# Optimization experiments

Measured on AMD Instinct MI355X. Metric: run time of the kernel, lower is better.

## Reference

```python
import jax, jax.numpy as jnp
import numpy as np

N = 100_000      # nodes
E = 400_000      # edges
NPERM = 100_000  # local receptive-field subgraphs
L = 16           # lrp_length
H = 64           # hid_dim
NLAYERS = 4
G = 1024         # graphs in the batch
P = NPERM * L    # permutation rows (must be NPERM * L)


def _spmm(row, col, val, mat, m):
    # COO sparse [m, n] @ dense [n, d]  (torch_sparse.spmm equivalent)
    return jax.ops.segment_sum(val[:, None] * mat[col], row, num_segments=m)


def setup_inputs() -> dict:
    key = jax.random.key(0)
    ks = jax.random.split(key, 16)
    inp = {}
    inp["node_feat"] = jax.random.normal(ks[0], (N, 28), jnp.float32)
    inp["degs"] = jax.random.uniform(ks[1], (N,), jnp.float32) * 8.0
    inp["batch"] = jnp.sort(jax.random.randint(ks[2], (N,), 0, G)).astype(jnp.int32)
    # node -> perm-length permutation matrix (one nonzero per perm row)
    inp["n2p_row"] = jnp.arange(P, dtype=jnp.int32)
    inp["n2p_col"] = jax.random.randint(ks[3], (P,), 0, N, dtype=jnp.int32)
    inp["n2p_val"] = jnp.ones((P,), jnp.float32)
    # edge -> perm-length permutation matrix
    inp["e2p_row"] = jnp.arange(P, dtype=jnp.int32)
    inp["e2p_col"] = jax.random.randint(ks[4], (P,), 0, E, dtype=jnp.int32)
    inp["e2p_val"] = jnp.ones((P,), jnp.float32)
    # pooling matrix: subgraph row -> root node, shape [N, NPERM]
    inp["pool_row"] = jax.random.randint(ks[5], (NPERM,), 0, N, dtype=jnp.int32)
    inp["pool_col"] = jnp.arange(NPERM, dtype=jnp.int32)
    inp["pool_val"] = jax.random.uniform(ks[6], (NPERM,), jnp.float32)
    # parameters
    inp["atom_W"] = jax.random.normal(ks[7], (28, H), jnp.float32) * 0.1
    inp["atom_b"] = jnp.zeros((H,), jnp.float32)
    inp["edge_W"] = jax.random.normal(ks[8], (1, H), jnp.float32) * 0.1
    inp["edge_b"] = jnp.zeros((H,), jnp.float32)
    inp["W_lrp"] = jax.random.normal(ks[9], (NLAYERS, H, H, L), jnp.float32) * 0.03
    inp["b_lrp"] = jnp.zeros((NLAYERS, H), jnp.float32)
    inp["dn0_W"] = jax.random.normal(ks[10], (NLAYERS, 1, 2 * H), jnp.float32) * 0.2
    inp["dn0_b"] = jnp.zeros((NLAYERS, 2 * H), jnp.float32)
    inp["dn1_W"] = jax.random.normal(ks[11], (NLAYERS, 2 * H, H), jnp.float32) * 0.1
    inp["dn1_b"] = jnp.zeros((NLAYERS, H), jnp.float32)
    return inp


def reference(node_feat, degs, batch,
              n2p_row, n2p_col, n2p_val,
              e2p_row, e2p_col, e2p_val,
              pool_row, pool_col, pool_val,
              atom_W, atom_b, edge_W, edge_b,
              W_lrp, b_lrp, dn0_W, dn0_b, dn1_W, dn1_b):
    x = node_feat @ atom_W + atom_b                       # atom_encoder  [N, H]
    # all edge features are 1 -> edge_encoder gives identical rows
    efeat = jnp.ones((E, 1), node_feat.dtype) @ edge_W + edge_b  # [E, H]
    for i in range(NLAYERS):
        # gather nodes + edges into perm-length layout   [P, H]
        perm = _spmm(n2p_row, n2p_col, n2p_val, x, P) \
             + _spmm(e2p_row, e2p_col, e2p_val, efeat, P)
        # transpose(0,1).view(H,-1,L).permute(1,2,0) == reshape(NPERM, L, H)
        t = perm.reshape(NPERM, L, H)
        # einsum('dab,bca->dc') with weights [H_in, H_out, L]
        h = jax.nn.relu(jnp.einsum('plh,hcl->pc', t, W_lrp[i]) + b_lrp[i])  # [NPERM, H]
        pooled = _spmm(pool_row, pool_col, pool_val, h, N)  # [N, H]
        hid = jax.nn.relu(degs[:, None] @ dn0_W[i] + dn0_b[i])  # [N, 2H]
        factor = hid @ dn1_W[i] + dn1_b[i]                      # [N, H]
        x = pooled * factor
    # global mean pool over graphs
    sums = jax.ops.segment_sum(x, batch, num_segments=G)
    cnts = jax.ops.segment_sum(jnp.ones((x.shape[0],), x.dtype), batch, num_segments=G)
    return sums / jnp.maximum(cnts, 1.0)[:, None]
```

## Files before the change

### kernel.cpp

```cpp
#include <hip/hip_runtime.h>

typedef __attribute__((ext_vector_type(8))) short bf16x8;
typedef __attribute__((ext_vector_type(4))) float f32x4;

#define N_NODES   100000
#define NPERM_    100000
#define L_        16
#define G_        1024
#define CAP_      20
#define OVF_MAX   4096

__device__ inline unsigned short f32_to_bf16(float f) {
    unsigned u = __float_as_uint(f);
    unsigned r = (u + 0x7fff + ((u >> 16) & 1)) >> 16;
    return (unsigned short)r;
}
__device__ inline float bflo(unsigned u) { return __uint_as_float(u << 16); }
__device__ inline float bfhi(unsigned u) { return __uint_as_float(u & 0xffff0000u); }
__device__ inline float bfup(unsigned short s) { return __uint_as_float((unsigned)s << 16); }
__device__ inline unsigned pk2(float a, float b) {
    return (unsigned)f32_to_bf16(a) | ((unsigned)f32_to_bf16(b) << 16);
}

typedef __attribute__((address_space(1))) const unsigned int gas_u32;
typedef __attribute__((address_space(3))) unsigned int las_u32;
__device__ __forceinline__ void gld16(const void* g, void* l) {
    __builtin_amdgcn_global_load_lds((gas_u32*)g, (las_u32*)l, 16, 0, 0);
}

__global__ __launch_bounds__(256) void k_prep_w(const float* __restrict__ W,
                                                unsigned short* __restrict__ Wt2) {
    int o = blockIdx.x * 256 + threadIdx.x;
    int j    = o & 7;
    int lane = (o >> 3) & 63;
    int sc   = (o >> 9) & 7;
    int l    = (o >> 12) & 15;
    int ho   = (o >> 16) & 1;
    int i    = o >> 17;
    int s = sc >> 2, cb = sc & 3;
    int k = s * 32 + (lane >> 4) * 8 + j;
    int c = cb * 16 + (lane & 15);
    float f = W[(((i * 64 + k) * 64) + c) * 16 + l];
    unsigned short hh = f32_to_bf16(f);
    Wt2[o] = ho ? f32_to_bf16(f - bfup(hh)) : hh;
}

__global__ __launch_bounds__(256) void k_prep_factor(const float* __restrict__ dn0_W,
                                                     const float* __restrict__ dn0_b,
                                                     const float* __restrict__ dn1_W,
                                                     const float* __restrict__ dn1_b,
                                                     float* __restrict__ tab,
                                                     float* __restrict__ thr) {
    int i     = blockIdx.x;
    int chunk = blockIdx.y;
    int tid   = threadIdx.x;
    __shared__ float A[128], B[128], ts[128], tv[128];
    __shared__ float W1l[128 * 64];
    if (tid < 128) { A[tid] = dn0_W[i * 128 + tid]; B[tid] = dn0_b[i * 128 + tid]; }
    {
        const float4* src = (const float4*)(dn1_W + (size_t)i * 8192);
        float4*       dst = (float4*)W1l;
        for (int t = tid; t < 2048; t += 256) dst[t] = src[t];
    }
    __syncthreads();
    if (tid < 128) {
        float a = A[tid], b = B[tid];
        float tj = -b / a;
        if (a == 0.f || !(tj > 0.f)) tj = 1e30f;
        tv[tid] = tj;
    }
    __syncthreads();
    if (tid < 128) {
        float tj = tv[tid];
        int rank = 0;
        for (int j = 0; j < 128; ++j) {
            float o = tv[j];
            rank += (o < tj) || (o == tj && j < tid);
        }
        ts[rank] = tj;
    }
    __syncthreads();
    if (chunk == 0 && tid < 128) thr[i * 128 + tid] = ts[tid];
    int s0 = chunk * 17;
    int s1 = min(s0 + 17, 129);
    float* tb = tab + (size_t)i * 129 * 128;
    for (int item = s0 * 64 + tid; item < s1 * 64; item += 256) {
        int s = item >> 6;
        int c = item & 63;
        float lo = (s == 0) ? 0.f : ts[s - 1];
        float hi = (s == 128) ? 1e30f : ts[s];
        float g;
        if (lo > 1e29f)       g = 1e29f;
        else if (hi > 1e29f)  g = lo + 1.f;
        else                  g = 0.5f * (lo + hi);
        float alpha = 0.f, beta = dn1_b[i * 64 + c];
        for (int j = 0; j < 128; ++j) {
            if (fmaf(g, A[j], B[j]) > 0.f) {
                float w1 = W1l[j * 64 + c];
                alpha = fmaf(A[j], w1, alpha);
                beta  = fmaf(B[j], w1, beta);
            }
        }
        tb[s * 128 + c * 2 + 0] = alpha;
        tb[s * 128 + c * 2 + 1] = beta;
    }
}

__global__ __launch_bounds__(256) void k_atom(const float* __restrict__ feat,
                                              const float* __restrict__ W,
                                              const float* __restrict__ b,
                                              unsigned short* __restrict__ xb) {
    __shared__ float Wlds[28 * 64];
    __shared__ float blds[64];
    int tid = threadIdx.x;
    for (int t = tid; t < 28 * 64; t += 256) Wlds[t] = W[t];
    if (tid < 64) blds[tid] = b[tid];
    __syncthreads();
    int n = blockIdx.x * 4 + (tid >> 6);
    int c = tid & 63;
    if (n >= N_NODES) return;
    const float* fr = feat + n * 28;
    float acc = blds[c];
#pragma unroll
    for (int j = 0; j < 28; ++j) acc = fmaf(fr[j], Wlds[j * 64 + c], acc);
    xb[n * 64 + c] = f32_to_bf16(acc);
}

__global__ __launch_bounds__(256) void k_bucket(const int* __restrict__ prow,
                                                int* __restrict__ cntn,
                                                int* __restrict__ bucket,
                                                int* __restrict__ ovf,
                                                int* __restrict__ ovfc) {
    int d = blockIdx.x * 256 + threadIdx.x;
    if (d >= NPERM_) return;
    int n = prow[d];
    int s = atomicAdd(cntn + n, 1);
    if (s < CAP_) bucket[n * CAP_ + s] = d;
    else { int o = atomicAdd(ovfc, 1); if (o < OVF_MAX) ovf[o] = d; }
}

__global__ __launch_bounds__(256, 3) void k_lrp(const unsigned short* __restrict__ xbuf,
                                                const int*   __restrict__ n2p_col,
                                                const float* __restrict__ n2p_val,
                                                const float* __restrict__ e2p_val,
                                                const float* __restrict__ edge_W,
                                                const float* __restrict__ edge_b,
                                                const unsigned short* __restrict__ Wt2,
                                                const float* __restrict__ bl,
                                                unsigned short* __restrict__ hout) {
    __shared__ unsigned short Tb[2][4][2][512];
    __shared__ unsigned short Wb[2][2][8][512];
    int tid = threadIdx.x;
    int lane = tid & 63;
    int w = tid >> 6;
    int r = lane & 15, q = lane >> 4;
    int d0 = blockIdx.x * 64;
    int myrow = w * 16 + r;
    int dg = min(d0 + myrow, NPERM_ - 1);
    size_t pbase = (size_t)dg * 16;

    float efr[2][8];
#pragma unroll
    for (int s = 0; s < 2; ++s) {
        int kb = s * 32 + q * 8;
        float4 wa = *(const float4*)(edge_W + kb);
        float4 wc = *(const float4*)(edge_W + kb + 4);
        float4 ba = *(const float4*)(edge_b + kb);
        float4 bc = *(const float4*)(edge_b + kb + 4);
        efr[s][0] = wa.x + ba.x; efr[s][1] = wa.y + ba.y;
        efr[s][2] = wa.z + ba.z; efr[s][3] = wa.w + ba.w;
        efr[s][4] = wc.x + bc.x; efr[s][5] = wc.y + bc.y;
        efr[s][6] = wc.z + bc.z; efr[s][7] = wc.w + bc.w;
    }

    f32x4 acc[4];
#pragma unroll
    for (int cb = 0; cb < 4; ++cb) acc[cb] = (f32x4)0.f;

    auto stage = [&](int l, int buf, int col) {
        const unsigned short* ap = xbuf + (size_t)col * 64 + q * 8;
        gld16(ap,      &Tb[buf][w][0][0]);
        gld16(ap + 32, &Tb[buf][w][1][0]);
        const unsigned short* wl = Wt2 + l * 4096;
#pragma unroll
        for (int i = 0; i < 4; ++i) {
            int c = w * 4 + i;
            gld16(wl + (c >> 3) * 65536 + (c & 7) * 512 + lane * 8,
                  &Wb[buf][c >> 3][c & 7][0]);
        }
    };

    int colA = n2p_col[pbase + 0];
    stage(0, 0, colA);
    colA = n2p_col[pbase + 1];
    float vnC = n2p_val[pbase + 0], veC = e2p_val[pbase + 0];
    __syncthreads();

#pragma unroll 1
    for (int l = 0; l < L_; ++l) {
        int buf = l & 1;
        if (l < 15) stage(l + 1, buf ^ 1, colA);
        if (l < 14) colA = n2p_col[pbase + l + 2];
        float vn = vnC, ve = veC;
        if (l < 15) { vnC = n2p_val[pbase + l + 1]; veC = e2p_val[pbase + l + 1]; }
#pragma unroll
        for (int s = 0; s < 2; ++s) {
            uint4 v = *(const uint4*)&Tb[buf][w][s][lane * 8];
            uint4 aw;
            aw.x = pk2(fmaf(vn, bflo(v.x), ve * efr[s][0]),
                       fmaf(vn, bfhi(v.x), ve * efr[s][1]));
            aw.y = pk2(fmaf(vn, bflo(v.y), ve * efr[s][2]),
                       fmaf(vn, bfhi(v.y), ve * efr[s][3]));
            aw.z = pk2(fmaf(vn, bflo(v.z), ve * efr[s][4]),
                       fmaf(vn, bfhi(v.z), ve * efr[s][5]));
            aw.w = pk2(fmaf(vn, bflo(v.w), ve * efr[s][6]),
                       fmaf(vn, bfhi(v.w), ve * efr[s][7]));
            bf16x8 a0 = *(bf16x8*)&aw;
#pragma unroll
            for (int cb = 0; cb < 4; ++cb) {
                bf16x8 bh = *(const bf16x8*)&Wb[buf][0][s * 4 + cb][lane * 8];
                bf16x8 bo = *(const bf16x8*)&Wb[buf][1][s * 4 + cb][lane * 8];
                acc[cb] = __builtin_amdgcn_mfma_f32_16x16x32_bf16(a0, bh, acc[cb], 0, 0, 0);
                acc[cb] = __builtin_amdgcn_mfma_f32_16x16x32_bf16(a0, bo, acc[cb], 0, 0, 0);
            }
        }
        __syncthreads();
    }

    {
        unsigned short* F = &Tb[0][0][0][0] + w * 1024;
#pragma unroll
        for (int cb = 0; cb < 4; ++cb) {
            float bias = bl[cb * 16 + r];
#pragma unroll
            for (int reg = 0; reg < 4; ++reg)
                F[(q * 4 + reg) * 64 + cb * 16 + r] =
                    f32_to_bf16(fmaxf(acc[cb][reg] + bias, 0.f));
        }
#pragma unroll
        for (int ii = 0; ii < 2; ++ii) {
            int idx = lane + ii * 64;
            uint4 v = ((const uint4*)F)[idx];
            int R = d0 + w * 16 + (idx >> 3);
            if (R < NPERM_)
                *(uint4*)(hout + (size_t)R * 64 + (idx & 7) * 8) = v;
        }
    }
}

__global__ __launch_bounds__(256) void k_pool_seg(const unsigned short* __restrict__ h,
                                                  const int*   __restrict__ cntn,
                                                  const int*   __restrict__ bucket,
                                                  const int*   __restrict__ ovf,
                                                  const int*   __restrict__ ovfc,
                                                  const int*   __restrict__ prow,
                                                  const float* __restrict__ pval,
                                                  const float* __restrict__ degs,
                                                  const float* __restrict__ tab,
                                                  const float* __restrict__ thr,
                                                  float* __restrict__ x,
                                                  unsigned short* __restrict__ xbo,
                                                  int last) {
    __shared__ float thrl[128];
    int tid = threadIdx.x;
    if (tid < 128) thrl[tid] = thr[tid];
    __syncthreads();
    int n  = blockIdx.x * 16 + (tid >> 4);
    int c4 = (tid & 15) * 4;
    if (n >= N_NODES) return;
    float dgv = degs[n];
    int seg = 0;
    if (thrl[63]       < dgv) seg = 64;
    if (thrl[seg + 31] < dgv) seg += 32;
    if (thrl[seg + 15] < dgv) seg += 16;
    if (thrl[seg + 7]  < dgv) seg += 8;
    if (thrl[seg + 3]  < dgv) seg += 4;
    if (thrl[seg + 1]  < dgv) seg += 2;
    if (thrl[seg]      < dgv) seg += 1;
    float4 p = make_float4(0.f, 0.f, 0.f, 0.f);
    int cn = min(cntn[n], CAP_);
    for (int j = 0; j < cn; ++j) {
        int   d  = bucket[n * CAP_ + j];
        float pv = pval[d];
        ushort4 hv = *(const ushort4*)(h + (size_t)d * 64 + c4);
        p.x = fmaf(pv, bfup(hv.x), p.x);
        p.y = fmaf(pv, bfup(hv.y), p.y);
        p.z = fmaf(pv, bfup(hv.z), p.z);
        p.w = fmaf(pv, bfup(hv.w), p.w);
    }
    int novf = *ovfc;
    if (novf > 0) {
        int ne = novf < OVF_MAX ? novf : OVF_MAX;
        for (int e = 0; e < ne; ++e) {
            int d = ovf[e];
            if (prow[d] == n) {
                float pv = pval[d];
                ushort4 hv = *(const ushort4*)(h + (size_t)d * 64 + c4);
                p.x = fmaf(pv, bfup(hv.x), p.x);
                p.y = fmaf(pv, bfup(hv.y), p.y);
                p.z = fmaf(pv, bfup(hv.z), p.z);
                p.w = fmaf(pv, bfup(hv.w), p.w);
            }
        }
    }
    const float4* tf = (const float4*)(tab + (size_t)(seg * 64 + c4) * 2);
    float4 t0 = tf[0], t1 = tf[1];
    float4 xo;
    xo.x = p.x * fmaf(t0.x, dgv, t0.y);
    xo.y = p.y * fmaf(t0.z, dgv, t0.w);
    xo.z = p.z * fmaf(t1.x, dgv, t1.y);
    xo.w = p.w * fmaf(t1.z, dgv, t1.w);
    if (last) {
        *(float4*)(x + (size_t)n * 64 + c4) = xo;
    } else {
        ushort4 s;
        s.x = f32_to_bf16(xo.x); s.y = f32_to_bf16(xo.y);
        s.z = f32_to_bf16(xo.z); s.w = f32_to_bf16(xo.w);
        *(ushort4*)(xbo + (size_t)n * 64 + c4) = s;
    }
}

__global__ __launch_bounds__(256) void k_gpool(const float* __restrict__ x,
                                               const int* __restrict__ batch,
                                               float* __restrict__ out,
                                               float* __restrict__ cnt) {
    int wave = (blockIdx.x * 256 + threadIdx.x) >> 6;
    int lane = threadIdx.x & 63;
    int n0 = wave * 64;
    if (n0 >= N_NODES) return;
    int n1 = min(n0 + 64, N_NODES);
    int g = batch[n0];
    float s = 0.f, c = 0.f;
    for (int n = n0; n < n1; ++n) {
        int gn = batch[n];
        if (gn != g) {
            atomicAdd(out + (size_t)g * 64 + lane, s);
            if (lane == 0) atomicAdd(cnt + g, c);
            s = 0.f; c = 0.f; g = gn;
        }
        s += x[(size_t)n * 64 + lane];
        c += 1.f;
    }
    atomicAdd(out + (size_t)g * 64 + lane, s);
    if (lane == 0) atomicAdd(cnt + g, c);
}

__global__ __launch_bounds__(256) void k_gdiv(float* __restrict__ out,
                                              const float* __restrict__ cnt) {
    int idx = blockIdx.x * 256 + threadIdx.x;
    if (idx >= G_ * 64) return;
    out[idx] /= fmaxf(cnt[idx >> 6], 1.f);
}

extern "C" void kernel_launch(void* const* d_in, const int* in_sizes, int n_in,
                              void* d_out, int out_size, void* d_ws, size_t ws_size,
                              hipStream_t stream) {
    const float* node_feat = (const float*)d_in[0];
    const float* degs      = (const float*)d_in[1];
    const int*   batch     = (const int*)  d_in[2];
    const int*   n2p_col   = (const int*)  d_in[4];
    const float* n2p_val   = (const float*)d_in[5];
    const float* e2p_val   = (const float*)d_in[8];
    const int*   pool_row  = (const int*)  d_in[9];
    const float* pool_val  = (const float*)d_in[11];
    const float* atom_W    = (const float*)d_in[12];
    const float* atom_b    = (const float*)d_in[13];
    const float* edge_W    = (const float*)d_in[14];
    const float* edge_b    = (const float*)d_in[15];
    const float* W_lrp     = (const float*)d_in[16];
    const float* b_lrp     = (const float*)d_in[17];
    const float* dn0_W     = (const float*)d_in[18];
    const float* dn0_b     = (const float*)d_in[19];
    const float* dn1_W     = (const float*)d_in[20];
    const float* dn1_b     = (const float*)d_in[21];

    char* ws = (char*)d_ws;
    unsigned short* h      = (unsigned short*)(ws);
    unsigned short* xb     = (unsigned short*)(ws + 12800000);
    unsigned short* Wt2    = (unsigned short*)(ws + 25600000);
    int*            bucket = (int*)           (ws + 26648576);
    int*            cntn   = (int*)           (ws + 34648576);
    int*            ovf    = (int*)           (ws + 35048576);
    int*            ovfc   = (int*)           (ws + 35064960);
    float*          tab    = (float*)         (ws + 35065088);
    float*          thr    = (float*)         (ws + 35329280);
    float*          cntg   = (float*)         (ws + 35331328);
    float*          x      = (float*)         (ws + 35335424);

    hipLaunchKernelGGL(k_prep_w, dim3(2048), dim3(256), 0, stream, W_lrp, Wt2);
    hipLaunchKernelGGL(k_prep_factor, dim3(4, 8), dim3(256), 0, stream,
                       dn0_W, dn0_b, dn1_W, dn1_b, tab, thr);
    hipLaunchKernelGGL(k_atom, dim3(25000), dim3(256), 0, stream,
                       node_feat, atom_W, atom_b, xb);
    hipMemsetAsync(cntn, 0, 416512, stream);
    hipLaunchKernelGGL(k_bucket, dim3(391), dim3(256), 0, stream,
                       pool_row, cntn, bucket, ovf, ovfc);
    for (int i = 0; i < 4; ++i) {
        hipLaunchKernelGGL(k_lrp, dim3(1563), dim3(256), 0, stream,
                           xb, n2p_col, n2p_val, e2p_val, edge_W, edge_b,
                           Wt2 + (size_t)i * 131072, b_lrp + i * 64, h);
        hipLaunchKernelGGL(k_pool_seg, dim3(6250), dim3(256), 0, stream,
                           h, cntn, bucket, ovf, ovfc, pool_row, pool_val,
                           degs, tab + (size_t)i * 129 * 128, thr + i * 128,
                           x, xb, (i == 3) ? 1 : 0);
    }
    hipMemsetAsync(d_out, 0, (size_t)G_ * 64 * 4, stream);
    hipMemsetAsync(cntg, 0, G_ * 4, stream);
    hipLaunchKernelGGL(k_gpool, dim3(391), dim3(256), 0, stream,
                       x, batch, (float*)d_out, cntg);
    hipLaunchKernelGGL(k_gdiv, dim3(256), dim3(256), 0, stream,
                       (float*)d_out, cntg);
}
```

Measured before the change: 675.9 us.

## Load LRP operands directly into registers instead of LDS double-buffering

The k_lrp kernel stops staging gathered node rows and weight tiles through LDS with global_load_lds and per-step barriers. Each lane now keeps two register prefetch buffers, two permutation steps ahead, and reads weight fragments straight from global memory, where they are expected to hit cache. This removes the __syncthreads per step and shrinks LDS use, which should allow higher occupancy now that the occupancy hint in launch_bounds is dropped. The cost is more register pressure and repeated per-wave global weight loads that could miss cache.

```diff
diff --git a/kernel.cpp b/kernel.cpp
--- a/kernel.cpp
+++ b/kernel.cpp
@@ -20,12 +20,6 @@
 __device__ inline float bfup(unsigned short s) { return __uint_as_float((unsigned)s << 16); }
 __device__ inline unsigned pk2(float a, float b) {
     return (unsigned)f32_to_bf16(a) | ((unsigned)f32_to_bf16(b) << 16);
-}
-
-typedef __attribute__((address_space(1))) const unsigned int gas_u32;
-typedef __attribute__((address_space(3))) unsigned int las_u32;
-__device__ __forceinline__ void gld16(const void* g, void* l) {
-    __builtin_amdgcn_global_load_lds((gas_u32*)g, (las_u32*)l, 16, 0, 0);
 }
 
 __global__ __launch_bounds__(256) void k_prep_w(const float* __restrict__ W,
@@ -139,24 +133,22 @@
     else { int o = atomicAdd(ovfc, 1); if (o < OVF_MAX) ovf[o] = d; }
 }
 
-__global__ __launch_bounds__(256, 3) void k_lrp(const unsigned short* __restrict__ xbuf,
-                                                const int*   __restrict__ n2p_col,
-                                                const float* __restrict__ n2p_val,
-                                                const float* __restrict__ e2p_val,
-                                                const float* __restrict__ edge_W,
-                                                const float* __restrict__ edge_b,
-                                                const unsigned short* __restrict__ Wt2,
-                                                const float* __restrict__ bl,
-                                                unsigned short* __restrict__ hout) {
-    __shared__ unsigned short Tb[2][4][2][512];
-    __shared__ unsigned short Wb[2][2][8][512];
+__global__ __launch_bounds__(256) void k_lrp(const unsigned short* __restrict__ xbuf,
+                                             const int*   __restrict__ n2p_col,
+                                             const float* __restrict__ n2p_val,
+                                             const float* __restrict__ e2p_val,
+                                             const float* __restrict__ edge_W,
+                                             const float* __restrict__ edge_b,
+                                             const unsigned short* __restrict__ Wt2,
+                                             const float* __restrict__ bl,
+                                             unsigned short* __restrict__ hout) {
+    __shared__ unsigned short Fb[4][1024];
     int tid = threadIdx.x;
     int lane = tid & 63;
     int w = tid >> 6;
     int r = lane & 15, q = lane >> 4;
     int d0 = blockIdx.x * 64;
-    int myrow = w * 16 + r;
-    int dg = min(d0 + myrow, NPERM_ - 1);
+    int dg = min(d0 + w * 16 + r, NPERM_ - 1);
     size_t pbase = (size_t)dg * 16;
 
     float efr[2][8];
@@ -177,58 +169,65 @@
 #pragma unroll
     for (int cb = 0; cb < 4; ++cb) acc[cb] = (f32x4)0.f;
 
-    auto stage = [&](int l, int buf, int col) {
-        const unsigned short* ap = xbuf + (size_t)col * 64 + q * 8;
-        gld16(ap,      &Tb[buf][w][0][0]);
-        gld16(ap + 32, &Tb[buf][w][1][0]);
-        const unsigned short* wl = Wt2 + l * 4096;
-#pragma unroll
-        for (int i = 0; i < 4; ++i) {
-            int c = w * 4 + i;
-            gld16(wl + (c >> 3) * 65536 + (c & 7) * 512 + lane * 8,
-                  &Wb[buf][c >> 3][c & 7][0]);
-        }
-    };
-
-    int colA = n2p_col[pbase + 0];
-    stage(0, 0, colA);
-    colA = n2p_col[pbase + 1];
-    float vnC = n2p_val[pbase + 0], veC = e2p_val[pbase + 0];
-    __syncthreads();
+    uint4 xvA[2], xvB[2];
+    int colN;
+    float vnC, veC;
+    {
+        int c0 = n2p_col[pbase + 0];
+        int c1 = n2p_col[pbase + 1];
+        const uint4* xr0 = (const uint4*)(xbuf + (size_t)c0 * 64 + q * 8);
+        xvA[0] = xr0[0]; xvA[1] = xr0[4];
+        const uint4* xr1 = (const uint4*)(xbuf + (size_t)c1 * 64 + q * 8);
+        xvB[0] = xr1[0]; xvB[1] = xr1[4];
+        colN = n2p_col[pbase + 2];
+        vnC = n2p_val[pbase + 0];
+        veC = e2p_val[pbase + 0];
+    }
+
+#define LRP_PHASE(LVAL, XV)                                                      \
+    {                                                                            \
+        const int l = (LVAL);                                                    \
+        float vn = vnC, ve = veC;                                                \
+        if (l < 15) { vnC = n2p_val[pbase + l + 1]; veC = e2p_val[pbase + l + 1]; } \
+        uint4 v0 = XV[0], v1 = XV[1];                                            \
+        if (l < 14) {             \
+            const uint4* xr = (const uint4*)(xbuf + (size_t)colN * 64 + q * 8);  \
+            XV[0] = xr[0]; XV[1] = xr[4];                                        \
+            if (l < 13) colN = n2p_col[pbase + l + 3];                           \
+        }                                                                        \
+        _Pragma("unroll")                                                        \
+        for (int s = 0; s < 2; ++s) {                                            \
+            uint4 v = s ? v1 : v0;                                               \
+            uint4 aw;                                                            \
+            aw.x = pk2(fmaf(vn, bflo(v.x), ve * efr[s][0]),                      \
+                       fmaf(vn, bfhi(v.x), ve * efr[s][1]));                     \
+            aw.y = pk2(fmaf(vn, bflo(v.y), ve * efr[s][2]),                      \
+                       fmaf(vn, bfhi(v.y), ve * efr[s][3]));                     \
+            aw.z = pk2(fmaf(vn, bflo(v.z), ve * efr[s][4]),                      \
+                       fmaf(vn, bfhi(v.z), ve * efr[s][5]));                     \
+            aw.w = pk2(fmaf(vn, bflo(v.w), ve * efr[s][6]),                      \
+                       fmaf(vn, bfhi(v.w), ve * efr[s][7]));                     \
+            bf16x8 a0 = *(bf16x8*)&aw;                                           \
+            const unsigned short* wp = Wt2 + l * 4096 + (s * 4) * 512 + lane * 8;\
+            _Pragma("unroll")                                                    \
+            for (int cb = 0; cb < 4; ++cb) {                                     \
+                bf16x8 bh = *(const bf16x8*)(wp + cb * 512);                     \
+                bf16x8 bo = *(const bf16x8*)(wp + 65536 + cb * 512);             \
+                acc[cb] = __builtin_amdgcn_mfma_f32_16x16x32_bf16(a0, bh, acc[cb], 0, 0, 0); \
+                acc[cb] = __builtin_amdgcn_mfma_f32_16x16x32_bf16(a0, bo, acc[cb], 0, 0, 0); \
+            }                                                                    \
+        }                                                                        \
+    }
 
 #pragma unroll 1
-    for (int l = 0; l < L_; ++l) {
-        int buf = l & 1;
-        if (l < 15) stage(l + 1, buf ^ 1, colA);
-        if (l < 14) colA = n2p_col[pbase + l + 2];
-        float vn = vnC, ve = veC;
-        if (l < 15) { vnC = n2p_val[pbase + l + 1]; veC = e2p_val[pbase + l + 1]; }
-#pragma unroll
-        for (int s = 0; s < 2; ++s) {
-            uint4 v = *(const uint4*)&Tb[buf][w][s][lane * 8];
-            uint4 aw;
-            aw.x = pk2(fmaf(vn, bflo(v.x), ve * efr[s][0]),
-                       fmaf(vn, bfhi(v.x), ve * efr[s][1]));
-            aw.y = pk2(fmaf(vn, bflo(v.y), ve * efr[s][2]),
-                       fmaf(vn, bfhi(v.y), ve * efr[s][3]));
-            aw.z = pk2(fmaf(vn, bflo(v.z), ve * efr[s][4]),
-                       fmaf(vn, bfhi(v.z), ve * efr[s][5]));
-            aw.w = pk2(fmaf(vn, bflo(v.w), ve * efr[s][6]),
-                       fmaf(vn, bfhi(v.w), ve * efr[s][7]));
-            bf16x8 a0 = *(bf16x8*)&aw;
-#pragma unroll
-            for (int cb = 0; cb < 4; ++cb) {
-                bf16x8 bh = *(const bf16x8*)&Wb[buf][0][s * 4 + cb][lane * 8];
-                bf16x8 bo = *(const bf16x8*)&Wb[buf][1][s * 4 + cb][lane * 8];
-                acc[cb] = __builtin_amdgcn_mfma_f32_16x16x32_bf16(a0, bh, acc[cb], 0, 0, 0);
-                acc[cb] = __builtin_amdgcn_mfma_f32_16x16x32_bf16(a0, bo, acc[cb], 0, 0, 0);
-            }
-        }
-        __syncthreads();
-    }
+    for (int lp = 0; lp < 8; ++lp) {
+        LRP_PHASE(2 * lp,     xvA)
+        LRP_PHASE(2 * lp + 1, xvB)
+    }
+#undef LRP_PHASE
 
     {
-        unsigned short* F = &Tb[0][0][0][0] + w * 1024;
+        unsigned short* F = &Fb[w][0];
 #pragma unroll
         for (int cb = 0; cb < 4; ++cb) {
             float bias = bl[cb * 16 + r];
```

After: 775.4 us. 14.7% more time.
